# Kernel optimization log

Hardware: AMD Instinct MI355X
Metric: run time of the kernel (lower is better)

The kernel has to match this reference:

```python
import jax, jax.numpy as jnp
import numpy as np

N_ENT = 200000; N_USR = 100000; D = 64
E = 1500000; NI = 1000000
HOPS = 2; N_ITER = 3; N_VIRT = 3; N_REL = 11
EPS = 1e-12


def setup_inputs() -> dict:
    key = jax.random.key(0)
    ks = jax.random.split(key, 8)
    entity_emb = jax.random.normal(ks[0], (N_ENT, D), jnp.float32) * 0.1
    user_emb = jax.random.normal(ks[1], (N_USR, D), jnp.float32) * 0.1
    latent_emb = jax.random.normal(ks[2], (N_VIRT, D), jnp.float32)
    rel_weight = jax.random.normal(ks[3], (N_REL - 1, D), jnp.float32)
    # per-hop Aggregator.w, initialized as in the module
    agg_w = jnp.tile(jnp.array([0.4, 0.3, 0.3], jnp.float32), (HOPS, 1))
    edge_index = jax.random.randint(ks[4], (2, E), 0, N_ENT)
    edge_type = jax.random.randint(ks[5], (E,), 1, N_REL)  # values in [1, n_relations-1]
    user_index = jax.random.randint(ks[6], (NI,), 0, N_USR)
    item_index = jax.random.randint(ks[7], (NI,), 0, N_ENT)
    return dict(entity_emb=entity_emb, user_emb=user_emb, latent_emb=latent_emb,
                rel_weight=rel_weight, agg_w=agg_w, edge_index=edge_index,
                edge_type=edge_type, user_index=user_index, item_index=item_index)


def _l2norm(x):
    n = jnp.linalg.norm(x, axis=1, keepdims=True)
    return x / jnp.maximum(n, EPS)


def _squash(u):
    sq = jnp.sum(u * u, axis=1, keepdims=True)  # ||u||^2
    return (sq / (sq + 1.0)) * _l2norm(u)


def _lws_entity(entity_emb, head, tail, mask_f):
    """LWS over a single virtual-relation edge subset (mask_f zeroes other edges).
    Matches torch: neigh is cumulatively sim-scaled across iterations."""
    cnt = jax.ops.segment_sum(mask_f, head, num_segments=N_ENT)
    denom = jnp.maximum(cnt, 1.0)[:, None]
    neigh = entity_emb[tail] * mask_f[:, None]          # [E, D]
    u = None
    for it in range(N_ITER):
        if u is not None:
            sim = jnp.sum(u[head] * neigh, axis=1, keepdims=True)
            neigh = sim * neigh
        u = jax.ops.segment_sum(neigh, head, num_segments=N_ENT) / denom
        if it < N_ITER - 1:
            u = _squash(u)
        u = u + entity_emb
    return u


def _lws_user(entity_emb, user_emb, user_index, item_index):
    """LWS for users; neigh is re-gathered fresh each iteration (as in torch)."""
    ones = jnp.ones((item_index.shape[0],), entity_emb.dtype)
    cnt = jax.ops.segment_sum(ones, user_index, num_segments=N_USR)
    denom = jnp.maximum(cnt, 1.0)[:, None]
    u = None
    for it in range(N_ITER):
        neigh = entity_emb[item_index]                  # [NI, D]
        if u is not None:
            sim = jnp.sum(u[user_index] * neigh, axis=1, keepdims=True)
            neigh = sim * neigh
        u = jax.ops.segment_sum(neigh, user_index, num_segments=N_USR) / denom
        if it < N_ITER - 1:
            u = _squash(u)
        u = u + user_emb
    return u


def reference(entity_emb, user_emb, latent_emb, rel_weight, agg_w,
              edge_index, edge_type, user_index, item_index):
    head, tail = edge_index[0], edge_index[1]
    # relation -> virtual-relation routing (argmax over similarity)
    relation_remap = jnp.argmax(rel_weight @ latent_emb.T, axis=1)   # [n_rel-1]
    et = relation_remap[edge_type - 1]                               # [E] in [0, N_VIRT)

    entity_res = entity_emb
    user_res = user_emb
    ent = entity_emb
    usr = user_emb
    for hop in range(HOPS):
        items = [_lws_entity(ent, head, tail, (et == i).astype(ent.dtype))
                 for i in range(N_VIRT)]
        w = jax.nn.softmax(agg_w[hop])                               # [3]
        entity_agg = w[0] * items[0] + w[1] * items[1] + w[2] * items[2]
        user_agg = _lws_user(ent, usr, user_index, item_index)
        # no dropout (eval mode); normalize + residual
        ent = _l2norm(entity_agg)
        usr = _l2norm(user_agg)
        entity_res = entity_res + ent
        user_res = user_res + usr
    return jnp.concatenate([entity_res, user_res], axis=0)          # [N_ENT+N_USR, D]
```

## Files before the change

### kernel.cpp

```cpp
#include <hip/hip_runtime.h>

#define N_ENT 200000
#define N_USR 100000
#define NT3   700000
#define UKEY0 600000
#define DIM 64
#define NE 1500000
#define NI_ 1000000
#define NTE 2500000
#define NREL1 10
#define NVIRT 3
#define EPSF 1e-12f
#define SCAN_B 1024
#define RE 6
#define RU 12

__device__ __forceinline__ float4 f4_zero() { return make_float4(0.f, 0.f, 0.f, 0.f); }
__device__ __forceinline__ float4 f4_add(float4 a, float4 b) {
    return make_float4(a.x + b.x, a.y + b.y, a.z + b.z, a.w + b.w);
}
__device__ __forceinline__ float4 f4_scale(float s, float4 a) {
    return make_float4(s * a.x, s * a.y, s * a.z, s * a.w);
}
__device__ __forceinline__ float4 f4_fma(float s, float4 a, float4 b) {
    return make_float4(fmaf(s, a.x, b.x), fmaf(s, a.y, b.y), fmaf(s, a.z, b.z), fmaf(s, a.w, b.w));
}
__device__ __forceinline__ float f4_dot(float4 a, float4 b) {
    return a.x * b.x + a.y * b.y + a.z * b.z + a.w * b.w;
}

__device__ __forceinline__ float red16(float v) {
    int x;
    x = __builtin_amdgcn_update_dpp(0, __float_as_int(v), 0xB1, 0xF, 0xF, true);
    v += __int_as_float(x);
    x = __builtin_amdgcn_update_dpp(0, __float_as_int(v), 0x4E, 0xF, 0xF, true);
    v += __int_as_float(x);
    x = __builtin_amdgcn_update_dpp(0, __float_as_int(v), 0x124, 0xF, 0xF, true);
    v += __int_as_float(x);
    x = __builtin_amdgcn_update_dpp(0, __float_as_int(v), 0x128, 0xF, 0xF, true);
    v += __int_as_float(x);
    return v;
}

__device__ __forceinline__ float4 squash4(float4 u, float sq) {
    float n = sqrtf(sq);
    float s = sq / ((sq + 1.f) * fmaxf(n, EPSF));
    return f4_scale(s, u);
}

__device__ __forceinline__ void block_remap(const float* __restrict__ rw,
                                            const float* __restrict__ lat,
                                            int* sremap) {
    int t = threadIdx.x;
    if (t < NREL1) {
        float best = -3.4e38f; int bi = 0;
        for (int j = 0; j < NVIRT; j++) {
            float s = 0.f;
            for (int d = 0; d < DIM; d++) s += rw[t * DIM + d] * lat[j * DIM + d];
            if (s > best) { best = s; bi = j; }
        }
        sremap[t] = bi;
    }
    __syncthreads();
}

__global__ void k_count_all(const int* __restrict__ head, const int* __restrict__ etype,
                            const float* __restrict__ rw, const float* __restrict__ lat,
                            const int* __restrict__ uidx, int* __restrict__ cnt) {
    __shared__ int sremap[NREL1];
    block_remap(rw, lat, sremap);
    int i = blockIdx.x * blockDim.x + threadIdx.x;
    if (i < NE) {
        int key = head[i] * 3 + sremap[etype[i] - 1];
        atomicAdd(&cnt[key], 1);
    } else if (i < NTE) {
        atomicAdd(&cnt[UKEY0 + uidx[i - NE]], 1);
    }
}

__global__ void k_scan1(const int* __restrict__ in, int* __restrict__ excl,
                        int* __restrict__ bsum, int n) {
    __shared__ int s[SCAN_B];
    int tid = threadIdx.x, gid = blockIdx.x * SCAN_B + tid;
    int v = (gid < n) ? in[gid] : 0;
    s[tid] = v; __syncthreads();
    for (int off = 1; off < SCAN_B; off <<= 1) {
        int t = 0;
        if (tid >= off) t = s[tid - off];
        __syncthreads();
        s[tid] += t;
        __syncthreads();
    }
    if (gid < n) excl[gid] = s[tid] - v;
    if (tid == SCAN_B - 1) bsum[blockIdx.x] = s[tid];
}

__global__ void k_scan23(const int* __restrict__ excl, const int* __restrict__ bsum,
                         const int* __restrict__ cnt, int* __restrict__ rp,
                         int* __restrict__ cur, int n, int nb) {
    __shared__ int s[SCAN_B];
    int tid = threadIdx.x;
    int v = (tid < nb && tid < (int)blockIdx.x) ? bsum[tid] : 0;
    s[tid] = v;
    __syncthreads();
    for (int off = SCAN_B / 2; off > 0; off >>= 1) {
        if (tid < off) s[tid] += s[tid + off];
        __syncthreads();
    }
    int prefix = s[0];
    int gid = blockIdx.x * SCAN_B + tid;
    if (gid < n) {
        int val = excl[gid] + prefix;
        rp[gid] = val;
        cur[gid] = val;
        if (gid == n - 1) rp[n] = val + cnt[gid];
    }
}

__global__ void k_scatter_all(const int* __restrict__ head, const int* __restrict__ tail,
                              const int* __restrict__ etype,
                              const float* __restrict__ rw, const float* __restrict__ lat,
                              const int* __restrict__ uidx, const int* __restrict__ iidx,
                              int* __restrict__ cur, int* __restrict__ sorted) {
    __shared__ int sremap[NREL1];
    block_remap(rw, lat, sremap);
    int i = blockIdx.x * blockDim.x + threadIdx.x;
    if (i < NE) {
        int key = head[i] * 3 + sremap[etype[i] - 1];
        int pos = atomicAdd(&cur[key], 1);
        sorted[pos] = tail[i];
    } else if (i < NTE) {
        int j = i - NE;
        int pos = atomicAdd(&cur[UKEY0 + uidx[j]], 1);
        sorted[pos] = iidx[j];
    }
}

#define NBLK_E (N_ENT / 16)
#define NBLK_U (N_USR / 16)

__global__ __launch_bounds__(256, 5) void k_hop(
    const float* __restrict__ ent, const float* __restrict__ usr,
    const int* __restrict__ rp, const int* __restrict__ sorted,
    const float* __restrict__ aw, int hop,
    float* __restrict__ ent_next, float* __restrict__ usr_next,
    int do_store, int first,
    float* __restrict__ outE, float* __restrict__ outU)
{
    int lane = threadIdx.x & 15;
    const float4* entv = (const float4*)ent;

    if (blockIdx.x < NBLK_E) {
        int g = blockIdx.x * 16 + (threadIdx.x >> 4);
        float4 eh = entv[g * 16 + lane];
        float4 agg = f4_zero();

        float a0 = aw[hop * 3 + 0], a1 = aw[hop * 3 + 1], a2 = aw[hop * 3 + 2];
        float m = fmaxf(a0, fmaxf(a1, a2));
        float e0 = expf(a0 - m), e1 = expf(a1 - m), e2 = expf(a2 - m);
        float esum = e0 + e1 + e2;
        float w0 = e0 / esum, w1 = e1 / esum, w2 = e2 / esum;

        int b3 = g * 3;
        int s0 = rp[b3], s1 = rp[b3 + 1], s2 = rp[b3 + 2], s3 = rp[b3 + 3];
        int dg0 = s1 - s0, dg1 = s2 - s1, dg2 = s3 - s2;
        int myp0 = (lane < dg0) ? sorted[s0 + lane] : 0;
        int myp1 = (lane < dg1) ? sorted[s1 + lane] : 0;
        int myp2 = (lane < dg2) ? sorted[s2 + lane] : 0;

        #pragma unroll
        for (int v = 0; v < NVIRT; v++) {
            int s   = (v == 0) ? s0   : (v == 1) ? s1   : s2;
            int deg = (v == 0) ? dg0  : (v == 1) ? dg1  : dg2;
            int myp = (v == 0) ? myp0 : (v == 1) ? myp1 : myp2;
            float w = (v == 0) ? w0   : (v == 1) ? w1   : w2;
            float inv = 1.f / fmaxf((float)deg, 1.f);

            float4 xc[RE];
            float4 acc = f4_zero();
            #pragma unroll
            for (int r = 0; r < RE; r++) {
                if (r < deg) {
                    int p = __shfl(myp, r, 16);
                    float4 x = entv[p * 16 + lane];
                    xc[r] = x;
                    acc = f4_add(acc, x);
                }
            }
            for (int r = RE; r < deg; r++) {
                int p = (r < 16) ? __shfl(myp, r, 16) : sorted[s + r];
                acc = f4_add(acc, entv[p * 16 + lane]);
            }
            float4 u = f4_scale(inv, acc);
            float sq = red16(f4_dot(u, u));
            float4 u1 = f4_add(squash4(u, sq), eh);

            float4 acc1 = f4_zero();
            float d1c[RE];
            float d1me = 0.f;
            #pragma unroll
            for (int r = 0; r < RE; r++) {
                if (r < deg) {
                    float4 x = xc[r];
                    float d1 = red16(f4_dot(u1, x));
                    d1c[r] = d1;
                    acc1 = f4_fma(d1, x, acc1);
                }
            }
            for (int r = RE; r < deg; r++) {
                int p = (r < 16) ? __shfl(myp, r, 16) : sorted[s + r];
                float4 x = entv[p * 16 + lane];
                float d1 = red16(f4_dot(u1, x));
                if (lane == r) d1me = d1;
                acc1 = f4_fma(d1, x, acc1);
            }
            u = f4_scale(inv, acc1);
            sq = red16(f4_dot(u, u));
            float4 u2 = f4_add(squash4(u, sq), eh);

            float4 acc2 = f4_zero();
            #pragma unroll
            for (int r = 0; r < RE; r++) {
                if (r < deg) {
                    float4 x = xc[r];
                    float d2 = red16(f4_dot(u2, x));
                    float d1 = d1c[r];
                    acc2 = f4_fma(d1 * d1 * d2, x, acc2);
                }
            }
            for (int r = RE; r < deg; r++) {
                int p = (r < 16) ? __shfl(myp, r, 16) : sorted[s + r];
                float4 x = entv[p * 16 + lane];
                float d2 = red16(f4_dot(u2, x));
                float d1 = (r < 16) ? __shfl(d1me, r, 16) : red16(f4_dot(u1, x));
                acc2 = f4_fma(d1 * d1 * d2, x, acc2);
            }
            agg = f4_fma(w * inv, acc2, agg);
        }
        agg = f4_add(agg, eh);
        float sq = red16(f4_dot(agg, agg));
        float nn = sqrtf(sq);
        float4 en = f4_scale(1.f / fmaxf(nn, EPSF), agg);
        if (do_store) ((float4*)ent_next)[g * 16 + lane] = en;
        float4* outv = (float4*)outE;
        float4 base = first ? eh : outv[g * 16 + lane];
        outv[g * 16 + lane] = f4_add(base, en);
    } else {
        int gu = (blockIdx.x - NBLK_E) * 16 + (threadIdx.x >> 4);
        int s = rp[UKEY0 + gu], e = rp[UKEY0 + gu + 1];
        int deg = e - s;
        const float4* usrv = (const float4*)usr;
        float4 uh = usrv[gu * 16 + lane];
        float inv = 1.f / fmaxf((float)deg, 1.f);

        int deg16 = (deg < 16) ? deg : 16;
        int myp = (lane < deg16) ? sorted[s + lane] : 0;

        float4 xc[RU];
        float4 acc = f4_zero();
        #pragma unroll
        for (int r = 0; r < RU; r++) {
            if (r < deg) {
                int p = __shfl(myp, r, 16);
                float4 x = entv[p * 16 + lane];
                xc[r] = x;
                acc = f4_add(acc, x);
            }
        }
        for (int r = RU; r < deg; r++) {
            int p = (r < 16) ? __shfl(myp, r, 16) : sorted[s + r];
            acc = f4_add(acc, entv[p * 16 + lane]);
        }
        float4 u = f4_scale(inv, acc);
        float sq = red16(f4_dot(u, u));
        float4 u1 = f4_add(squash4(u, sq), uh);

        acc = f4_zero();
        #pragma unroll
        for (int r = 0; r < RU; r++) {
            if (r < deg) {
                float4 x = xc[r];
                acc = f4_fma(red16(f4_dot(u1, x)), x, acc);
            }
        }
        for (int r = RU; r < deg; r++) {
            int p = (r < 16) ? __shfl(myp, r, 16) : sorted[s + r];
            float4 x = entv[p * 16 + lane];
            acc = f4_fma(red16(f4_dot(u1, x)), x, acc);
        }
        u = f4_scale(inv, acc);
        sq = red16(f4_dot(u, u));
        float4 u2 = f4_add(squash4(u, sq), uh);

        acc = f4_zero();
        #pragma unroll
        for (int r = 0; r < RU; r++) {
            if (r < deg) {
                float4 x = xc[r];
                acc = f4_fma(red16(f4_dot(u2, x)), x, acc);
            }
        }
        for (int r = RU; r < deg; r++) {
            int p = (r < 16) ? __shfl(myp, r, 16) : sorted[s + r];
            float4 x = entv[p * 16 + lane];
            acc = f4_fma(red16(f4_dot(u2, x)), x, acc);
        }
        float4 u3 = f4_add(f4_scale(inv, acc), uh);
        sq = red16(f4_dot(u3, u3));
        float nn = sqrtf(sq);
        float4 un = f4_scale(1.f / fmaxf(nn, EPSF), u3);
        if (do_store) ((float4*)usr_next)[gu * 16 + lane] = un;
        float4* outv = (float4*)outU;
        float4 base = first ? uh : outv[gu * 16 + lane];
        outv[gu * 16 + lane] = f4_add(base, un);
    }
}

extern "C" void kernel_launch(void* const* d_in, const int* in_sizes, int n_in,
                              void* d_out, int out_size, void* d_ws, size_t ws_size,
                              hipStream_t stream)
{
    const float* entity_emb = (const float*)d_in[0];
    const float* user_emb   = (const float*)d_in[1];
    const float* latent     = (const float*)d_in[2];
    const float* rel_w      = (const float*)d_in[3];
    const float* agg_w      = (const float*)d_in[4];
    const int* edge_index   = (const int*)d_in[5];
    const int* edge_type    = (const int*)d_in[6];
    const int* user_index   = (const int*)d_in[7];
    const int* item_index   = (const int*)d_in[8];
    float* out = (float*)d_out;

    char* ws = (char*)d_ws;
    size_t off = 0;
    auto alloc = [&](size_t bytes) -> void* {
        void* p = ws + off;
        off += (bytes + 255) / 256 * 256;
        return p;
    };
    float* entA  = (float*)alloc((size_t)N_ENT * DIM * 4);
    float* usrA  = (float*)alloc((size_t)N_USR * DIM * 4);
    int* cnt     = (int*)alloc((size_t)NT3 * 4);
    int* rp      = (int*)alloc((size_t)(NT3 + 1) * 4);
    int* cur     = (int*)alloc((size_t)NT3 * 4);
    int* excl    = (int*)alloc((size_t)NT3 * 4);
    int* bsum    = (int*)alloc(1024 * 4);
    int* sorted  = (int*)alloc((size_t)NTE * 4);

    const int* head = edge_index;
    const int* tail = edge_index + NE;

    hipMemsetAsync(cnt, 0, (size_t)NT3 * 4, stream);

    k_count_all<<<(NTE + 255) / 256, 256, 0, stream>>>(
        head, edge_type, rel_w, latent, user_index, cnt);

    int nb = (NT3 + SCAN_B - 1) / SCAN_B;
    k_scan1<<<nb, SCAN_B, 0, stream>>>(cnt, excl, bsum, NT3);
    k_scan23<<<nb, SCAN_B, 0, stream>>>(excl, bsum, cnt, rp, cur, NT3, nb);

    k_scatter_all<<<(NTE + 255) / 256, 256, 0, stream>>>(
        head, tail, edge_type, rel_w, latent, user_index, item_index, cur, sorted);

    const float* ec = entity_emb;
    const float* uc = user_emb;
    for (int hop = 0; hop < 2; hop++) {
        int do_store = (hop == 0);
        int first = (hop == 0);
        k_hop<<<NBLK_E + NBLK_U, 256, 0, stream>>>(
            ec, uc, rp, sorted, agg_w, hop, entA, usrA, do_store, first,
            out, out + (size_t)N_ENT * DIM);
        ec = entA;
        uc = usrA;
    }
}
```

Measured before the change: 771.0 us.

## Sort entities and users by degree to balance work across wavefront groups

Adds a degree histogram, a bucket scan and a permutation build so that each 16-lane group in the hop kernel handles nodes with similar degree. The goal is less divergence and imbalance inside waves and blocks, where one high-degree node stalls the rest. In exchange it adds three small kernels, atomic contention on a 64-bucket histogram, and an indirection that scatters the node-row reads and output writes, which hurts coalescing and locality.

```diff
diff --git a/kernel.cpp b/kernel.cpp
--- a/kernel.cpp
+++ b/kernel.cpp
@@ -14,6 +14,7 @@
 #define SCAN_B 1024
 #define RE 6
 #define RU 12
+#define NBUCK 64
 
 __device__ __forceinline__ float4 f4_zero() { return make_float4(0.f, 0.f, 0.f, 0.f); }
 __device__ __forceinline__ float4 f4_add(float4 a, float4 b) {
@@ -136,12 +137,57 @@
     }
 }
 
+__global__ void k_deghist(const int* __restrict__ rp, int* __restrict__ hist) {
+    int i = blockIdx.x * blockDim.x + threadIdx.x;
+    if (i < N_ENT) {
+        int d = rp[i * 3 + 3] - rp[i * 3];
+        atomicAdd(&hist[min(d, NBUCK - 1)], 1);
+    } else if (i < N_ENT + N_USR) {
+        int u = i - N_ENT;
+        int d = rp[UKEY0 + u + 1] - rp[UKEY0 + u];
+        atomicAdd(&hist[NBUCK + min(d, NBUCK - 1)], 1);
+    }
+}
+
+__global__ void k_bucketscan(int* __restrict__ hist) {
+    __shared__ int sE[NBUCK], sU[NBUCK];
+    int t = threadIdx.x;
+    int hE = hist[t], hU = hist[NBUCK + t];
+    sE[t] = hE; sU[t] = hU;
+    __syncthreads();
+    for (int off = 1; off < NBUCK; off <<= 1) {
+        int vE = 0, vU = 0;
+        if (t >= off) { vE = sE[t - off]; vU = sU[t - off]; }
+        __syncthreads();
+        sE[t] += vE; sU[t] += vU;
+        __syncthreads();
+    }
+    hist[128 + t] = sE[t] - hE;
+    hist[192 + t] = sU[t] - hU;
+}
+
+__global__ void k_permbuild(const int* __restrict__ rp, int* __restrict__ hist,
+                            int* __restrict__ permE, int* __restrict__ permU) {
+    int i = blockIdx.x * blockDim.x + threadIdx.x;
+    if (i < N_ENT) {
+        int d = rp[i * 3 + 3] - rp[i * 3];
+        int pos = atomicAdd(&hist[128 + min(d, NBUCK - 1)], 1);
+        permE[pos] = i;
+    } else if (i < N_ENT + N_USR) {
+        int u = i - N_ENT;
+        int d = rp[UKEY0 + u + 1] - rp[UKEY0 + u];
+        int pos = atomicAdd(&hist[192 + min(d, NBUCK - 1)], 1);
+        permU[pos] = u;
+    }
+}
+
 #define NBLK_E (N_ENT / 16)
 #define NBLK_U (N_USR / 16)
 
 __global__ __launch_bounds__(256, 5) void k_hop(
     const float* __restrict__ ent, const float* __restrict__ usr,
     const int* __restrict__ rp, const int* __restrict__ sorted,
+    const int* __restrict__ permE, const int* __restrict__ permU,
     const float* __restrict__ aw, int hop,
     float* __restrict__ ent_next, float* __restrict__ usr_next,
     int do_store, int first,
@@ -151,7 +197,7 @@
     const float4* entv = (const float4*)ent;
 
     if (blockIdx.x < NBLK_E) {
-        int g = blockIdx.x * 16 + (threadIdx.x >> 4);
+        int g = permE[blockIdx.x * 16 + (threadIdx.x >> 4)];
         float4 eh = entv[g * 16 + lane];
         float4 agg = f4_zero();
 
@@ -246,7 +292,7 @@
         float4 base = first ? eh : outv[g * 16 + lane];
         outv[g * 16 + lane] = f4_add(base, en);
     } else {
-        int gu = (blockIdx.x - NBLK_E) * 16 + (threadIdx.x >> 4);
+        int gu = permU[(blockIdx.x - NBLK_E) * 16 + (threadIdx.x >> 4)];
         int s = rp[UKEY0 + gu], e = rp[UKEY0 + gu + 1];
         int deg = e - s;
         const float4* usrv = (const float4*)usr;
@@ -346,11 +392,15 @@
     int* excl    = (int*)alloc((size_t)NT3 * 4);
     int* bsum    = (int*)alloc(1024 * 4);
     int* sorted  = (int*)alloc((size_t)NTE * 4);
+    int* hist    = (int*)alloc(256 * 4);
+    int* permE   = (int*)alloc((size_t)N_ENT * 4);
+    int* permU   = (int*)alloc((size_t)N_USR * 4);
 
     const int* head = edge_index;
     const int* tail = edge_index + NE;
 
     hipMemsetAsync(cnt, 0, (size_t)NT3 * 4, stream);
+    hipMemsetAsync(hist, 0, 256 * 4, stream);
 
     k_count_all<<<(NTE + 255) / 256, 256, 0, stream>>>(
         head, edge_type, rel_w, latent, user_index, cnt);
@@ -361,6 +411,11 @@
 
     k_scatter_all<<<(NTE + 255) / 256, 256, 0, stream>>>(
         head, tail, edge_type, rel_w, latent, user_index, item_index, cur, sorted);
+
+    int npg = (N_ENT + N_USR + 255) / 256;
+    k_deghist<<<npg, 256, 0, stream>>>(rp, hist);
+    k_bucketscan<<<1, NBUCK, 0, stream>>>(hist);
+    k_permbuild<<<npg, 256, 0, stream>>>(rp, hist, permE, permU);
 
     const float* ec = entity_emb;
     const float* uc = user_emb;
@@ -368,7 +423,7 @@
         int do_store = (hop == 0);
         int first = (hop == 0);
         k_hop<<<NBLK_E + NBLK_U, 256, 0, stream>>>(
-            ec, uc, rp, sorted, agg_w, hop, entA, usrA, do_store, first,
+            ec, uc, rp, sorted, permE, permU, agg_w, hop, entA, usrA, do_store, first,
             out, out + (size_t)N_ENT * DIM);
         ec = entA;
         uc = usrA;
```

New measurement: 2.441 ms. +216.6%, slower.

## Sort entity and user nodes by degree to balance per-wave work in hop kernel

Applied to the files above, without the earlier changes.

Adds a stable counting sort of entities and users into degree buckets (histogram, per-bucket scan, bucket base, permutation scatter). The hop kernel then processes nodes in permuted order, so each 16-lane group within a wave handles nodes of similar degree, which reduces divergence and idle lanes from uneven degree loops. The cost is four extra small kernels plus scattered row access to embeddings and outputs, which loses the sequential locality of the original order.

```diff
diff --git a/kernel.cpp b/kernel.cpp
--- a/kernel.cpp
+++ b/kernel.cpp
@@ -14,6 +14,9 @@
 #define SCAN_B 1024
 #define RE 6
 #define RU 12
+#define NBUCK 64
+#define NPERM (N_ENT + N_USR)
+#define NPB   ((NPERM + 255) / 256)
 
 __device__ __forceinline__ float4 f4_zero() { return make_float4(0.f, 0.f, 0.f, 0.f); }
 __device__ __forceinline__ float4 f4_add(float4 a, float4 b) {
@@ -136,12 +139,89 @@
     }
 }
 
+__device__ __forceinline__ int perm_bucket(const int* __restrict__ rp, int i) {
+    if (i < N_ENT) {
+        int d = rp[i * 3 + 3] - rp[i * 3];
+        return (d < NBUCK) ? d : (NBUCK - 1);
+    }
+    int u = i - N_ENT;
+    int d = rp[UKEY0 + u + 1] - rp[UKEY0 + u];
+    return NBUCK + ((d < NBUCK) ? d : (NBUCK - 1));
+}
+
+__global__ void k_histL(const int* __restrict__ rp, int* __restrict__ bh) {
+    __shared__ int h[2 * NBUCK];
+    int t = threadIdx.x;
+    if (t < 2 * NBUCK) h[t] = 0;
+    __syncthreads();
+    int i = blockIdx.x * 256 + t;
+    if (i < NPERM) atomicAdd(&h[perm_bucket(rp, i)], 1);
+    __syncthreads();
+    if (t < 2 * NBUCK) bh[t * NPB + blockIdx.x] = h[t];
+}
+
+__global__ void k_histscan(int* __restrict__ bh, int* __restrict__ bt) {
+    __shared__ int s[SCAN_B];
+    int b = blockIdx.x, t = threadIdx.x;
+    int base = b * NPB;
+    int i0 = 2 * t, i1 = 2 * t + 1;
+    int a0 = (i0 < NPB) ? bh[base + i0] : 0;
+    int a1 = (i1 < NPB) ? bh[base + i1] : 0;
+    int pair = a0 + a1;
+    s[t] = pair; __syncthreads();
+    for (int off = 1; off < SCAN_B; off <<= 1) {
+        int v = 0;
+        if (t >= off) v = s[t - off];
+        __syncthreads();
+        s[t] += v;
+        __syncthreads();
+    }
+    int exclPair = s[t] - pair;
+    if (i0 < NPB) bh[base + i0] = exclPair;
+    if (i1 < NPB) bh[base + i1] = exclPair + a0;
+    if (t == SCAN_B - 1) bt[b] = s[t];
+}
+
+__global__ void k_bucketbase(const int* __restrict__ bt, int* __restrict__ bb) {
+    __shared__ int s[2 * NBUCK];
+    int t = threadIdx.x;
+    int v = bt[t];
+    s[t] = v;
+    __syncthreads();
+    for (int off = 1; off < NBUCK; off <<= 1) {
+        int x = 0;
+        if (t >= off && ((t - off) >> 6) == (t >> 6)) x = s[t - off];
+        __syncthreads();
+        s[t] += x;
+        __syncthreads();
+    }
+    bb[t] = s[t] - v;
+}
+
+__global__ void k_permb(const int* __restrict__ rp, const int* __restrict__ bh,
+                        const int* __restrict__ bb,
+                        int* __restrict__ permE, int* __restrict__ permU) {
+    __shared__ int cur[2 * NBUCK];
+    int t = threadIdx.x;
+    if (t < 2 * NBUCK) cur[t] = 0;
+    __syncthreads();
+    int i = blockIdx.x * 256 + t;
+    if (i < NPERM) {
+        int b = perm_bucket(rp, i);
+        int l = atomicAdd(&cur[b], 1);
+        int pos = bb[b] + bh[b * NPB + blockIdx.x] + l;
+        if (i < N_ENT) permE[pos] = i;
+        else permU[pos] = i - N_ENT;
+    }
+}
+
 #define NBLK_E (N_ENT / 16)
 #define NBLK_U (N_USR / 16)
 
 __global__ __launch_bounds__(256, 5) void k_hop(
     const float* __restrict__ ent, const float* __restrict__ usr,
     const int* __restrict__ rp, const int* __restrict__ sorted,
+    const int* __restrict__ permE, const int* __restrict__ permU,
     const float* __restrict__ aw, int hop,
     float* __restrict__ ent_next, float* __restrict__ usr_next,
     int do_store, int first,
@@ -151,7 +231,7 @@
     const float4* entv = (const float4*)ent;
 
     if (blockIdx.x < NBLK_E) {
-        int g = blockIdx.x * 16 + (threadIdx.x >> 4);
+        int g = permE[blockIdx.x * 16 + (threadIdx.x >> 4)];
         float4 eh = entv[g * 16 + lane];
         float4 agg = f4_zero();
 
@@ -246,7 +326,7 @@
         float4 base = first ? eh : outv[g * 16 + lane];
         outv[g * 16 + lane] = f4_add(base, en);
     } else {
-        int gu = (blockIdx.x - NBLK_E) * 16 + (threadIdx.x >> 4);
+        int gu = permU[(blockIdx.x - NBLK_E) * 16 + (threadIdx.x >> 4)];
         int s = rp[UKEY0 + gu], e = rp[UKEY0 + gu + 1];
         int deg = e - s;
         const float4* usrv = (const float4*)usr;
@@ -346,6 +426,11 @@
     int* excl    = (int*)alloc((size_t)NT3 * 4);
     int* bsum    = (int*)alloc(1024 * 4);
     int* sorted  = (int*)alloc((size_t)NTE * 4);
+    int* bh      = (int*)alloc((size_t)2 * NBUCK * NPB * 4);
+    int* bt      = (int*)alloc(2 * NBUCK * 4);
+    int* bb      = (int*)alloc(2 * NBUCK * 4);
+    int* permE   = (int*)alloc((size_t)N_ENT * 4);
+    int* permU   = (int*)alloc((size_t)N_USR * 4);
 
     const int* head = edge_index;
     const int* tail = edge_index + NE;
@@ -361,6 +446,11 @@
 
     k_scatter_all<<<(NTE + 255) / 256, 256, 0, stream>>>(
         head, tail, edge_type, rel_w, latent, user_index, item_index, cur, sorted);
+
+    k_histL<<<NPB, 256, 0, stream>>>(rp, bh);
+    k_histscan<<<2 * NBUCK, SCAN_B, 0, stream>>>(bh, bt);
+    k_bucketbase<<<1, 2 * NBUCK, 0, stream>>>(bt, bb);
+    k_permb<<<NPB, 256, 0, stream>>>(rp, bh, bb, permE, permU);
 
     const float* ec = entity_emb;
     const float* uc = user_emb;
@@ -368,7 +458,7 @@
         int do_store = (hop == 0);
         int first = (hop == 0);
         k_hop<<<NBLK_E + NBLK_U, 256, 0, stream>>>(
-            ec, uc, rp, sorted, agg_w, hop, entA, usrA, do_store, first,
+            ec, uc, rp, sorted, permE, permU, agg_w, hop, entA, usrA, do_store, first,
             out, out + (size_t)N_ENT * DIM);
         ec = entA;
         uc = usrA;
```

New measurement: 741.3 us. 1.04x faster.
